# Kernel tuning notes

Hardware: AMD Instinct MI355X
Metric: run time of the kernel (lower is better)

## Reference

```python
import jax, jax.numpy as jnp
import numpy as np

B, LQ, LKV, D, DV = 8, 2048, 2048, 128, 128


def setup_inputs() -> dict:
    key = jax.random.key(0)
    kq, kk, kv = jax.random.split(key, 3)
    return {
        "query": jax.random.normal(kq, (B, LQ, D), dtype=jnp.float32),
        "key": jax.random.normal(kk, (B, LKV, D), dtype=jnp.float32),
        "value": jax.random.normal(kv, (B, LKV, DV), dtype=jnp.float32),
    }


def reference(query, key, value):
    # score_fn: scaled dot-product  score = Q K^T / sqrt(Dq)
    scale = 1.0 / jnp.sqrt(jnp.asarray(query.shape[-1], query.dtype))
    score = jnp.einsum("bqd,bkd->bqk", query, key) * scale  # (B, Lq, Lkv)
    attention_weights = jax.nn.softmax(score, axis=-1)
    context_vector = jnp.einsum("bqk,bkv->bqv", attention_weights, value)
    return attention_weights, context_vector
```

## Files before the change

kernel.cpp:

```cpp
#include <hip/hip_runtime.h>

#define BB    8
#define LQN   2048
#define LKVN  2048
#define DQ    128
#define DVN   128
#define QT    16
#define KT    64
#define KSTR  136
#define VSTR  72
#define PSTR  72
#define NT    (LKVN / KT)

typedef short short8 __attribute__((ext_vector_type(8)));
typedef float f32x4  __attribute__((ext_vector_type(4)));

__device__ __forceinline__ short f2bf(float f) {
  unsigned u = __builtin_bit_cast(unsigned, f);
  u += 0x7fffu + ((u >> 16) & 1u);
  return (short)(u >> 16);
}

__global__ __launch_bounds__(256) void conv_kernel(const float* __restrict__ Q,
                                                   const float* __restrict__ K,
                                                   short* __restrict__ Qb,
                                                   short* __restrict__ Kb) {
  int i = blockIdx.x * 256 + threadIdx.x;
  const float* s; short* d;
  if (i < 262144) { s = Q; d = Qb; }
  else            { s = K; d = Kb; i -= 262144; }
  size_t off = (size_t)i * 8;
  float4 a = *(const float4*)(s + off);
  float4 b = *(const float4*)(s + off + 4);
  short8 o;
  o[0] = f2bf(a.x); o[1] = f2bf(a.y); o[2] = f2bf(a.z); o[3] = f2bf(a.w);
  o[4] = f2bf(b.x); o[5] = f2bf(b.y); o[6] = f2bf(b.z); o[7] = f2bf(b.w);
  *(short8*)(d + off) = o;
}

__global__ __launch_bounds__(256) void vtrans_kernel(const float* __restrict__ V,
                                                     short* __restrict__ Vt) {
  __shared__ float tile[128][33];
  const int kv0 = blockIdx.x * 128;
  const int dv0 = blockIdx.y * 32;
  const int b   = blockIdx.z;
  const int tid = threadIdx.x;
  const float* src = V + ((size_t)b * LKVN + kv0) * DVN + dv0;
#pragma unroll
  for (int it = 0; it < 4; ++it) {
    int idx = it * 256 + tid;
    int r = idx >> 3, c4 = idx & 7;
    float4 v = *(const float4*)(src + (size_t)r * DVN + c4 * 4);
    tile[r][c4 * 4 + 0] = v.x;
    tile[r][c4 * 4 + 1] = v.y;
    tile[r][c4 * 4 + 2] = v.z;
    tile[r][c4 * 4 + 3] = v.w;
  }
  __syncthreads();
  short* dst = Vt + ((size_t)b * DVN + dv0) * LKVN + kv0;
#pragma unroll
  for (int it = 0; it < 2; ++it) {
    int idx = it * 256 + tid;
    int row = idx >> 4, ch = idx & 15;
    short8 o;
#pragma unroll
    for (int j = 0; j < 8; ++j) o[j] = f2bf(tile[ch * 8 + j][row]);
    *(short8*)(dst + (size_t)row * LKVN + ch * 8) = o;
  }
}

__global__ __launch_bounds__(256, 4) void attn_kernel(const short* __restrict__ Qb,
                                                      const short* __restrict__ Kb,
                                                      const short* __restrict__ Vt,
                                                      float* __restrict__ W,
                                                      float* __restrict__ O) {
  __shared__ __align__(16) short k_lds[KT][KSTR];
  __shared__ __align__(16) short v_lds[DVN][VSTR];
  __shared__ __align__(16) short p_lds[QT][PSTR];
  __shared__ float red_l[4][QT];
  __shared__ float stats_r[QT];

  const int tid  = threadIdx.x;
  const int w    = tid >> 6;
  const int lane = tid & 63;
  const int n    = lane & 15;
  const int qd   = lane >> 4;
  const int b    = blockIdx.x & 7;
  const int q0   = (blockIdx.x >> 3) * QT;

  const short* Kbase = Kb + (size_t)b * LKVN * DQ;
  const short* Vbase = Vt + (size_t)b * DVN * LKVN;

  const int kr = tid >> 4, kc = tid & 15;
  const int vr = tid >> 3, vc = tid & 7;

  short8 qf[4];
  {
    const short* Qrow = Qb + ((size_t)b * LQN + q0 + n) * DQ + qd * 8;
#pragma unroll
    for (int ks = 0; ks < 4; ++ks) qf[ks] = *(const short8*)(Qrow + ks * 32);
  }

  const float scale = 0.08838834764831845f;
  float l_part[4] = {0.f, 0.f, 0.f, 0.f};
  short8 kreg[4], vreg[4];

#pragma unroll
  for (int it = 0; it < 4; ++it)
    kreg[it] = *(const short8*)(Kbase + (size_t)(kr + it * 16) * DQ + kc * 8);
#pragma unroll
  for (int it = 0; it < 4; ++it)
    *(short8*)&k_lds[kr + it * 16][kc * 8] = kreg[it];

  for (int t = 0; t < NT; ++t) {
    __syncthreads();
    if (t + 1 < NT) {
      const short* src = Kbase + (size_t)(t + 1) * KT * DQ;
#pragma unroll
      for (int it = 0; it < 4; ++it)
        kreg[it] = *(const short8*)(src + (size_t)(kr + it * 16) * DQ + kc * 8);
    }
    f32x4 acc = {0.f, 0.f, 0.f, 0.f};
#pragma unroll
    for (int ks = 0; ks < 4; ++ks) {
      short8 bf = *(const short8*)&k_lds[w * 16 + n][ks * 32 + qd * 8];
      acc = __builtin_amdgcn_mfma_f32_16x16x32_bf16(qf[ks], bf, acc, 0, 0, 0);
    }
#pragma unroll
    for (int r = 0; r < 4; ++r) l_part[r] += __expf(acc[r] * scale);
    __syncthreads();
    if (t + 1 < NT) {
#pragma unroll
      for (int it = 0; it < 4; ++it)
        *(short8*)&k_lds[kr + it * 16][kc * 8] = kreg[it];
    }
  }

#pragma unroll
  for (int r = 0; r < 4; ++r)
#pragma unroll
    for (int off = 1; off < 16; off <<= 1)
      l_part[r] += __shfl_xor(l_part[r], off, 64);
  if (n == 0)
#pragma unroll
    for (int r = 0; r < 4; ++r) red_l[w][qd * 4 + r] = l_part[r];
  __syncthreads();
  if (tid < QT)
    stats_r[tid] = 1.0f / (red_l[0][tid] + red_l[1][tid] + red_l[2][tid] + red_l[3][tid]);
  __syncthreads();
  float rinv[4];
#pragma unroll
  for (int r = 0; r < 4; ++r) rinv[r] = stats_r[qd * 4 + r];

  f32x4 oacc[2];
  oacc[0] = (f32x4){0.f, 0.f, 0.f, 0.f};
  oacc[1] = (f32x4){0.f, 0.f, 0.f, 0.f};
  float* Wb = W + ((size_t)b * LQN + q0) * LKVN;

#pragma unroll
  for (int it = 0; it < 4; ++it)
    kreg[it] = *(const short8*)(Kbase + (size_t)(kr + it * 16) * DQ + kc * 8);
#pragma unroll
  for (int it = 0; it < 4; ++it)
    vreg[it] = *(const short8*)(Vbase + (size_t)(vr + it * 32) * LKVN + vc * 8);
#pragma unroll
  for (int it = 0; it < 4; ++it)
    *(short8*)&k_lds[kr + it * 16][kc * 8] = kreg[it];
#pragma unroll
  for (int it = 0; it < 4; ++it)
    *(short8*)&v_lds[vr + it * 32][vc * 8] = vreg[it];

  for (int t = 0; t < NT; ++t) {
    const int kv0 = t * KT;
    __syncthreads();
    if (t + 1 < NT) {
      const short* ksrc = Kbase + (size_t)(kv0 + KT) * DQ;
      const short* vsrc = Vbase + kv0 + KT;
#pragma unroll
      for (int it = 0; it < 4; ++it)
        kreg[it] = *(const short8*)(ksrc + (size_t)(kr + it * 16) * DQ + kc * 8);
#pragma unroll
      for (int it = 0; it < 4; ++it)
        vreg[it] = *(const short8*)(vsrc + (size_t)(vr + it * 32) * LKVN + vc * 8);
    }
    f32x4 acc = {0.f, 0.f, 0.f, 0.f};
#pragma unroll
    for (int ks = 0; ks < 4; ++ks) {
      short8 bf = *(const short8*)&k_lds[w * 16 + n][ks * 32 + qd * 8];
      acc = __builtin_amdgcn_mfma_f32_16x16x32_bf16(qf[ks], bf, acc, 0, 0, 0);
    }
    float p[4];
#pragma unroll
    for (int r = 0; r < 4; ++r) p[r] = __expf(acc[r] * scale) * rinv[r];
#pragma unroll
    for (int r = 0; r < 4; ++r)
      Wb[(size_t)(qd * 4 + r) * LKVN + kv0 + w * 16 + n] = p[r];
#pragma unroll
    for (int r = 0; r < 4; ++r) p_lds[qd * 4 + r][w * 16 + n] = f2bf(p[r]);
    __syncthreads();
    short8 pa0 = *(const short8*)&p_lds[n][qd * 8];
    short8 pa1 = *(const short8*)&p_lds[n][32 + qd * 8];
#pragma unroll
    for (int c = 0; c < 2; ++c) {
      const int dv = w * 32 + c * 16 + n;
      short8 b0 = *(const short8*)&v_lds[dv][qd * 8];
      short8 b1 = *(const short8*)&v_lds[dv][32 + qd * 8];
      oacc[c] = __builtin_amdgcn_mfma_f32_16x16x32_bf16(pa0, b0, oacc[c], 0, 0, 0);
      oacc[c] = __builtin_amdgcn_mfma_f32_16x16x32_bf16(pa1, b1, oacc[c], 0, 0, 0);
    }
    __syncthreads();
    if (t + 1 < NT) {
#pragma unroll
      for (int it = 0; it < 4; ++it)
        *(short8*)&k_lds[kr + it * 16][kc * 8] = kreg[it];
#pragma unroll
      for (int it = 0; it < 4; ++it)
        *(short8*)&v_lds[vr + it * 32][vc * 8] = vreg[it];
    }
  }

  float* Ob = O + ((size_t)b * LQN + q0) * DVN;
#pragma unroll
  for (int c = 0; c < 2; ++c)
#pragma unroll
    for (int r = 0; r < 4; ++r)
      Ob[(size_t)(qd * 4 + r) * DVN + w * 32 + c * 16 + n] = oacc[c][r];
}

extern "C" void kernel_launch(void* const* d_in, const int* in_sizes, int n_in,
                              void* d_out, int out_size, void* d_ws, size_t ws_size,
                              hipStream_t stream) {
  const float* Q = (const float*)d_in[0];
  const float* K = (const float*)d_in[1];
  const float* V = (const float*)d_in[2];
  float* W = (float*)d_out;
  float* O = W + (size_t)BB * LQN * LKVN;
  short* Qb = (short*)d_ws;
  short* Kb = Qb + (size_t)BB * LQN * DQ;
  short* Vt = Kb + (size_t)BB * LKVN * DQ;

  conv_kernel<<<2048, 256, 0, stream>>>(Q, K, Qb, Kb);
  vtrans_kernel<<<dim3(LKVN / 128, DVN / 32, BB), 256, 0, stream>>>(V, Vt);
  attn_kernel<<<1024, 256, 0, stream>>>(Qb, Kb, Vt, W, O);
}
```

Measured before the change: 224.3 us.

## Restructure attention to split KV across waves with register-direct K/V loads

The attention kernel now processes 32 query rows per block, and each wave owns a 32-wide slice of every 128-wide KV tile. K and V fragments are loaded straight from global memory into registers, with double buffering in the first pass, instead of being staged through LDS behind block barriers. The probability fragments are reshuffled between lanes with shuffles rather than a shared-memory round trip, W is written as vector stores, and the per-wave partial outputs are reduced through LDS at the end. Q conversion moves into the attention kernel and the K-convert and V-transpose kernels are merged into one launch. The changes aim to cut barrier and LDS traffic and launch count, but they raise register pressure (launch bounds drop to 2), halve the grid to 512 blocks, and drop LDS reuse of K/V across waves.

```diff
diff --git a/kernel.cpp b/kernel.cpp
--- a/kernel.cpp
+++ b/kernel.cpp
@@ -5,15 +5,15 @@
 #define LKVN  2048
 #define DQ    128
 #define DVN   128
-#define QT    16
-#define KT    64
-#define KSTR  136
-#define VSTR  72
-#define PSTR  72
-#define NT    (LKVN / KT)
+#define QT    32
+#define KVW   32
+#define KTI   128
+#define NT    (LKVN / KTI)
+#define OSTR  132
 
 typedef short short8 __attribute__((ext_vector_type(8)));
 typedef float f32x4  __attribute__((ext_vector_type(4)));
+typedef int   int4v  __attribute__((ext_vector_type(4)));
 
 __device__ __forceinline__ short f2bf(float f) {
   unsigned u = __builtin_bit_cast(unsigned, f);
@@ -21,29 +21,32 @@
   return (short)(u >> 16);
 }
 
-__global__ __launch_bounds__(256) void conv_kernel(const float* __restrict__ Q,
-                                                   const float* __restrict__ K,
-                                                   short* __restrict__ Qb,
-                                                   short* __restrict__ Kb) {
-  int i = blockIdx.x * 256 + threadIdx.x;
-  const float* s; short* d;
-  if (i < 262144) { s = Q; d = Qb; }
-  else            { s = K; d = Kb; i -= 262144; }
-  size_t off = (size_t)i * 8;
-  float4 a = *(const float4*)(s + off);
-  float4 b = *(const float4*)(s + off + 4);
-  short8 o;
-  o[0] = f2bf(a.x); o[1] = f2bf(a.y); o[2] = f2bf(a.z); o[3] = f2bf(a.w);
-  o[4] = f2bf(b.x); o[5] = f2bf(b.y); o[6] = f2bf(b.z); o[7] = f2bf(b.w);
-  *(short8*)(d + off) = o;
-}
-
-__global__ __launch_bounds__(256) void vtrans_kernel(const float* __restrict__ V,
-                                                     short* __restrict__ Vt) {
+__device__ __forceinline__ int packbf(float a, float b) {
+  unsigned lo = (unsigned short)f2bf(a);
+  unsigned hi = (unsigned short)f2bf(b);
+  return (int)(lo | (hi << 16));
+}
+
+__global__ __launch_bounds__(256) void pre_kernel(const float* __restrict__ K,
+                                                  const float* __restrict__ V,
+                                                  short* __restrict__ Kb,
+                                                  short* __restrict__ Vt) {
   __shared__ float tile[128][33];
-  const int kv0 = blockIdx.x * 128;
-  const int dv0 = blockIdx.y * 32;
-  const int b   = blockIdx.z;
+  if (blockIdx.x >= 512) {
+    int i = (blockIdx.x - 512) * 256 + threadIdx.x;
+    size_t off = (size_t)i * 8;
+    float4 a = *(const float4*)(K + off);
+    float4 c = *(const float4*)(K + off + 4);
+    short8 o;
+    o[0] = f2bf(a.x); o[1] = f2bf(a.y); o[2] = f2bf(a.z); o[3] = f2bf(a.w);
+    o[4] = f2bf(c.x); o[5] = f2bf(c.y); o[6] = f2bf(c.z); o[7] = f2bf(c.w);
+    *(short8*)(Kb + off) = o;
+    return;
+  }
+  const int bx  = blockIdx.x;
+  const int kv0 = (bx & 15) * 128;
+  const int dv0 = ((bx >> 4) & 3) * 32;
+  const int b   = bx >> 6;
   const int tid = threadIdx.x;
   const float* src = V + ((size_t)b * LKVN + kv0) * DVN + dv0;
 #pragma unroll
@@ -69,16 +72,88 @@
   }
 }
 
-__global__ __launch_bounds__(256, 4) void attn_kernel(const short* __restrict__ Qb,
+#define P1_BODY(kc, kn, t)                                                          \
+  {                                                                                 \
+    if ((t) + 1 < NT) {                                                             \
+      _Pragma("unroll")                                                             \
+      for (int t2 = 0; t2 < 2; ++t2)                                                \
+        _Pragma("unroll")                                                           \
+        for (int ks = 0; ks < 4; ++ks)                                              \
+          kn[t2 * 4 + ks] =                                                         \
+              *(const short8*)(Kw + ((size_t)(((t) + 1) * KTI + t2 * 16)) * DQ + ks * 32); \
+    }                                                                               \
+    _Pragma("unroll")                                                               \
+    for (int g = 0; g < 2; ++g)                                                     \
+      _Pragma("unroll")                                                             \
+      for (int t2 = 0; t2 < 2; ++t2) {                                              \
+        f32x4 acc = {0.f, 0.f, 0.f, 0.f};                                           \
+        _Pragma("unroll")                                                           \
+        for (int ks = 0; ks < 4; ++ks)                                              \
+          acc = __builtin_amdgcn_mfma_f32_16x16x32_bf16(kc[t2 * 4 + ks], qf[g][ks], acc, 0, 0, 0); \
+        _Pragma("unroll")                                                           \
+        for (int r = 0; r < 4; ++r) l_part[g] += __expf(acc[r] * scale);            \
+      }                                                                             \
+  }
+
+#define P2_BODY(t)                                                                  \
+  {                                                                                 \
+    _Pragma("unroll")                                                               \
+    for (int t2 = 0; t2 < 2; ++t2)                                                  \
+      _Pragma("unroll")                                                             \
+      for (int ks = 0; ks < 4; ++ks)                                                \
+        kA[t2 * 4 + ks] =                                                           \
+            *(const short8*)(Kw + ((size_t)((t) * KTI + t2 * 16)) * DQ + ks * 32);  \
+    short8 vf[8];                                                                   \
+    _Pragma("unroll")                                                               \
+    for (int dvg = 0; dvg < 8; ++dvg)                                               \
+      vf[dvg] = *(const short8*)(Vw + (size_t)(dvg * 16) * LKVN + (t) * KTI);       \
+    int pk[2][2][2];                                                                \
+    _Pragma("unroll")                                                               \
+    for (int g = 0; g < 2; ++g)                                                     \
+      _Pragma("unroll")                                                             \
+      for (int t2 = 0; t2 < 2; ++t2) {                                              \
+        f32x4 acc = {0.f, 0.f, 0.f, 0.f};                                           \
+        _Pragma("unroll")                                                           \
+        for (int ks = 0; ks < 4; ++ks)                                              \
+          acc = __builtin_amdgcn_mfma_f32_16x16x32_bf16(kA[t2 * 4 + ks], qf[g][ks], acc, 0, 0, 0); \
+        float p0 = __expf(acc[0] * scale) * rinv[g];                                \
+        float p1 = __expf(acc[1] * scale) * rinv[g];                                \
+        float p2 = __expf(acc[2] * scale) * rinv[g];                                \
+        float p3 = __expf(acc[3] * scale) * rinv[g];                                \
+        f32x4 st = {p0, p1, p2, p3};                                                \
+        *(f32x4*)(Wrow + (size_t)(g * 16) * LKVN + (t) * KTI + t2 * 16) = st;       \
+        pk[g][t2][0] = packbf(p0, p1);                                              \
+        pk[g][t2][1] = packbf(p2, p3);                                              \
+      }                                                                             \
+    _Pragma("unroll")                                                               \
+    for (int g = 0; g < 2; ++g) {                                                   \
+      int a0 = __shfl(pk[g][0][0], srcA, 64);                                       \
+      int b0 = __shfl(pk[g][1][0], srcA, 64);                                       \
+      int a1 = __shfl(pk[g][0][1], srcA, 64);                                       \
+      int b1 = __shfl(pk[g][1][1], srcA, 64);                                       \
+      int a2 = __shfl(pk[g][0][0], srcB, 64);                                       \
+      int b2 = __shfl(pk[g][1][0], srcB, 64);                                       \
+      int a3 = __shfl(pk[g][0][1], srcB, 64);                                       \
+      int b3 = __shfl(pk[g][1][1], srcB, 64);                                       \
+      int4v bi;                                                                     \
+      bi[0] = sel ? b0 : a0;                                                        \
+      bi[1] = sel ? b1 : a1;                                                        \
+      bi[2] = sel ? b2 : a2;                                                        \
+      bi[3] = sel ? b3 : a3;                                                        \
+      short8 bfr = __builtin_bit_cast(short8, bi);                                  \
+      _Pragma("unroll")                                                             \
+      for (int dvg = 0; dvg < 8; ++dvg)                                             \
+        oacc[g][dvg] = __builtin_amdgcn_mfma_f32_16x16x32_bf16(vf[dvg], bfr, oacc[g][dvg], 0, 0, 0); \
+    }                                                                               \
+  }
+
+__global__ __launch_bounds__(256, 2) void attn_kernel(const float* __restrict__ Q,
                                                       const short* __restrict__ Kb,
                                                       const short* __restrict__ Vt,
                                                       float* __restrict__ W,
                                                       float* __restrict__ O) {
-  __shared__ __align__(16) short k_lds[KT][KSTR];
-  __shared__ __align__(16) short v_lds[DVN][VSTR];
-  __shared__ __align__(16) short p_lds[QT][PSTR];
+  __shared__ __align__(16) float osum[2][QT][OSTR];
   __shared__ float red_l[4][QT];
-  __shared__ float stats_r[QT];
 
   const int tid  = threadIdx.x;
   const int w    = tid >> 6;
@@ -88,143 +163,100 @@
   const int b    = blockIdx.x & 7;
   const int q0   = (blockIdx.x >> 3) * QT;
 
-  const short* Kbase = Kb + (size_t)b * LKVN * DQ;
-  const short* Vbase = Vt + (size_t)b * DVN * LKVN;
-
-  const int kr = tid >> 4, kc = tid & 15;
-  const int vr = tid >> 3, vc = tid & 7;
-
-  short8 qf[4];
-  {
-    const short* Qrow = Qb + ((size_t)b * LQN + q0 + n) * DQ + qd * 8;
-#pragma unroll
-    for (int ks = 0; ks < 4; ++ks) qf[ks] = *(const short8*)(Qrow + ks * 32);
+  const short* Kw = Kb + ((size_t)b * LKVN + w * KVW + n) * DQ + qd * 8;
+  const short* Vw = Vt + ((size_t)b * DVN + n) * LKVN + w * KVW + qd * 8;
+  float* Wrow = W + ((size_t)b * LQN + q0 + n) * LKVN + w * KVW + qd * 4;
+
+  short8 qf[2][4];
+#pragma unroll
+  for (int g = 0; g < 2; ++g) {
+    const float* Qrow = Q + ((size_t)b * LQN + q0 + g * 16 + n) * DQ + qd * 8;
+#pragma unroll
+    for (int ks = 0; ks < 4; ++ks) {
+      float4 f0 = *(const float4*)(Qrow + ks * 32);
+      float4 f1 = *(const float4*)(Qrow + ks * 32 + 4);
+      short8 o;
+      o[0] = f2bf(f0.x); o[1] = f2bf(f0.y); o[2] = f2bf(f0.z); o[3] = f2bf(f0.w);
+      o[4] = f2bf(f1.x); o[5] = f2bf(f1.y); o[6] = f2bf(f1.z); o[7] = f2bf(f1.w);
+      qf[g][ks] = o;
+    }
   }
 
   const float scale = 0.08838834764831845f;
-  float l_part[4] = {0.f, 0.f, 0.f, 0.f};
-  short8 kreg[4], vreg[4];
-
-#pragma unroll
-  for (int it = 0; it < 4; ++it)
-    kreg[it] = *(const short8*)(Kbase + (size_t)(kr + it * 16) * DQ + kc * 8);
-#pragma unroll
-  for (int it = 0; it < 4; ++it)
-    *(short8*)&k_lds[kr + it * 16][kc * 8] = kreg[it];
+  float l_part[2] = {0.f, 0.f};
+
+  short8 kA[8], kB[8];
+#pragma unroll
+  for (int t2 = 0; t2 < 2; ++t2)
+#pragma unroll
+    for (int ks = 0; ks < 4; ++ks)
+      kA[t2 * 4 + ks] = *(const short8*)(Kw + ((size_t)(t2 * 16)) * DQ + ks * 32);
+
+  for (int t = 0; t < NT; t += 2) {
+    P1_BODY(kA, kB, t)
+    P1_BODY(kB, kA, t + 1)
+  }
+
+#pragma unroll
+  for (int g = 0; g < 2; ++g) {
+    l_part[g] += __shfl_xor(l_part[g], 16, 64);
+    l_part[g] += __shfl_xor(l_part[g], 32, 64);
+  }
+  if (lane < 16) {
+    red_l[w][lane]      = l_part[0];
+    red_l[w][16 + lane] = l_part[1];
+  }
+  __syncthreads();
+  float rinv[2];
+#pragma unroll
+  for (int g = 0; g < 2; ++g) {
+    int qq = g * 16 + n;
+    rinv[g] = 1.0f / (red_l[0][qq] + red_l[1][qq] + red_l[2][qq] + red_l[3][qq]);
+  }
+
+  const int srcA = n + ((qd & 1) << 5);
+  const int srcB = srcA + 16;
+  const int sel  = qd >> 1;
+
+  f32x4 oacc[2][8];
+#pragma unroll
+  for (int g = 0; g < 2; ++g)
+#pragma unroll
+    for (int dvg = 0; dvg < 8; ++dvg) oacc[g][dvg] = (f32x4){0.f, 0.f, 0.f, 0.f};
 
   for (int t = 0; t < NT; ++t) {
-    __syncthreads();
-    if (t + 1 < NT) {
-      const short* src = Kbase + (size_t)(t + 1) * KT * DQ;
-#pragma unroll
-      for (int it = 0; it < 4; ++it)
-        kreg[it] = *(const short8*)(src + (size_t)(kr + it * 16) * DQ + kc * 8);
-    }
-    f32x4 acc = {0.f, 0.f, 0.f, 0.f};
-#pragma unroll
-    for (int ks = 0; ks < 4; ++ks) {
-      short8 bf = *(const short8*)&k_lds[w * 16 + n][ks * 32 + qd * 8];
-      acc = __builtin_amdgcn_mfma_f32_16x16x32_bf16(qf[ks], bf, acc, 0, 0, 0);
-    }
-#pragma unroll
-    for (int r = 0; r < 4; ++r) l_part[r] += __expf(acc[r] * scale);
-    __syncthreads();
-    if (t + 1 < NT) {
-#pragma unroll
-      for (int it = 0; it < 4; ++it)
-        *(short8*)&k_lds[kr + it * 16][kc * 8] = kreg[it];
-    }
-  }
-
-#pragma unroll
-  for (int r = 0; r < 4; ++r)
-#pragma unroll
-    for (int off = 1; off < 16; off <<= 1)
-      l_part[r] += __shfl_xor(l_part[r], off, 64);
-  if (n == 0)
-#pragma unroll
-    for (int r = 0; r < 4; ++r) red_l[w][qd * 4 + r] = l_part[r];
-  __syncthreads();
-  if (tid < QT)
-    stats_r[tid] = 1.0f / (red_l[0][tid] + red_l[1][tid] + red_l[2][tid] + red_l[3][tid]);
-  __syncthreads();
-  float rinv[4];
-#pragma unroll
-  for (int r = 0; r < 4; ++r) rinv[r] = stats_r[qd * 4 + r];
-
-  f32x4 oacc[2];
-  oacc[0] = (f32x4){0.f, 0.f, 0.f, 0.f};
-  oacc[1] = (f32x4){0.f, 0.f, 0.f, 0.f};
-  float* Wb = W + ((size_t)b * LQN + q0) * LKVN;
-
-#pragma unroll
-  for (int it = 0; it < 4; ++it)
-    kreg[it] = *(const short8*)(Kbase + (size_t)(kr + it * 16) * DQ + kc * 8);
-#pragma unroll
-  for (int it = 0; it < 4; ++it)
-    vreg[it] = *(const short8*)(Vbase + (size_t)(vr + it * 32) * LKVN + vc * 8);
-#pragma unroll
-  for (int it = 0; it < 4; ++it)
-    *(short8*)&k_lds[kr + it * 16][kc * 8] = kreg[it];
-#pragma unroll
-  for (int it = 0; it < 4; ++it)
-    *(short8*)&v_lds[vr + it * 32][vc * 8] = vreg[it];
-
-  for (int t = 0; t < NT; ++t) {
-    const int kv0 = t * KT;
-    __syncthreads();
-    if (t + 1 < NT) {
-      const short* ksrc = Kbase + (size_t)(kv0 + KT) * DQ;
-      const short* vsrc = Vbase + kv0 + KT;
-#pragma unroll
-      for (int it = 0; it < 4; ++it)
-        kreg[it] = *(const short8*)(ksrc + (size_t)(kr + it * 16) * DQ + kc * 8);
-#pragma unroll
-      for (int it = 0; it < 4; ++it)
-        vreg[it] = *(const short8*)(vsrc + (size_t)(vr + it * 32) * LKVN + vc * 8);
-    }
-    f32x4 acc = {0.f, 0.f, 0.f, 0.f};
-#pragma unroll
-    for (int ks = 0; ks < 4; ++ks) {
-      short8 bf = *(const short8*)&k_lds[w * 16 + n][ks * 32 + qd * 8];
-      acc = __builtin_amdgcn_mfma_f32_16x16x32_bf16(qf[ks], bf, acc, 0, 0, 0);
-    }
-    float p[4];
-#pragma unroll
-    for (int r = 0; r < 4; ++r) p[r] = __expf(acc[r] * scale) * rinv[r];
-#pragma unroll
-    for (int r = 0; r < 4; ++r)
-      Wb[(size_t)(qd * 4 + r) * LKVN + kv0 + w * 16 + n] = p[r];
-#pragma unroll
-    for (int r = 0; r < 4; ++r) p_lds[qd * 4 + r][w * 16 + n] = f2bf(p[r]);
-    __syncthreads();
-    short8 pa0 = *(const short8*)&p_lds[n][qd * 8];
-    short8 pa1 = *(const short8*)&p_lds[n][32 + qd * 8];
-#pragma unroll
-    for (int c = 0; c < 2; ++c) {
-      const int dv = w * 32 + c * 16 + n;
-      short8 b0 = *(const short8*)&v_lds[dv][qd * 8];
-      short8 b1 = *(const short8*)&v_lds[dv][32 + qd * 8];
-      oacc[c] = __builtin_amdgcn_mfma_f32_16x16x32_bf16(pa0, b0, oacc[c], 0, 0, 0);
-      oacc[c] = __builtin_amdgcn_mfma_f32_16x16x32_bf16(pa1, b1, oacc[c], 0, 0, 0);
-    }
-    __syncthreads();
-    if (t + 1 < NT) {
-#pragma unroll
-      for (int it = 0; it < 4; ++it)
-        *(short8*)&k_lds[kr + it * 16][kc * 8] = kreg[it];
-#pragma unroll
-      for (int it = 0; it < 4; ++it)
-        *(short8*)&v_lds[vr + it * 32][vc * 8] = vreg[it];
-    }
-  }
+    P2_BODY(t)
+  }
+
+  if (w < 2) {
+#pragma unroll
+    for (int g = 0; g < 2; ++g)
+#pragma unroll
+      for (int dvg = 0; dvg < 8; ++dvg)
+        *(f32x4*)&osum[w][g * 16 + n][dvg * 16 + qd * 4] = oacc[g][dvg];
+  }
+  __syncthreads();
+  if (w >= 2) {
+#pragma unroll
+    for (int g = 0; g < 2; ++g)
+#pragma unroll
+      for (int dvg = 0; dvg < 8; ++dvg) {
+        f32x4* p = (f32x4*)&osum[w - 2][g * 16 + n][dvg * 16 + qd * 4];
+        *p = *p + oacc[g][dvg];
+      }
+  }
+  __syncthreads();
 
   float* Ob = O + ((size_t)b * LQN + q0) * DVN;
-#pragma unroll
-  for (int c = 0; c < 2; ++c)
-#pragma unroll
-    for (int r = 0; r < 4; ++r)
-      Ob[(size_t)(qd * 4 + r) * DVN + w * 32 + c * 16 + n] = oacc[c][r];
+  const int qq = tid >> 3;
+  const int c0 = (tid & 7) * 16;
+#pragma unroll
+  for (int c = 0; c < 4; ++c) {
+    f32x4 s = *(const f32x4*)&osum[0][qq][c0 + c * 4];
+    f32x4 s1 = *(const f32x4*)&osum[1][qq][c0 + c * 4];
+    s = s + s1;
+    *(f32x4*)(Ob + (size_t)qq * DVN + c0 + c * 4) = s;
+  }
 }
 
 extern "C" void kernel_launch(void* const* d_in, const int* in_sizes, int n_in,
@@ -235,11 +267,9 @@
   const float* V = (const float*)d_in[2];
   float* W = (float*)d_out;
   float* O = W + (size_t)BB * LQN * LKVN;
-  short* Qb = (short*)d_ws;
-  short* Kb = Qb + (size_t)BB * LQN * DQ;
+  short* Kb = (short*)d_ws;
   short* Vt = Kb + (size_t)BB * LKVN * DQ;
 
-  conv_kernel<<<2048, 256, 0, stream>>>(Q, K, Qb, Kb);
-  vtrans_kernel<<<dim3(LKVN / 128, DVN / 32, BB), 256, 0, stream>>>(V, Vt);
-  attn_kernel<<<1024, 256, 0, stream>>>(Qb, Kb, Vt, W, O);
-}
+  pre_kernel<<<1536, 256, 0, stream>>>(K, V, Kb, Vt);
+  attn_kernel<<<512, 256, 0, stream>>>(Q, Kb, Vt, W, O);
+}
```

Measured after the change: 233.5 us. +4.1%, slower.
